# Kernel tuning notes

Measured on AMD Instinct MI355X. Metric: run time of the kernel, lower is better.

Reference implementation:

```python
import jax, jax.numpy as jnp
import numpy as np

B, T, V, EMB, H = 16, 128, 32000, 512, 512
PAD = 0


def setup_inputs() -> dict:
    key = jax.random.key(0)
    ks = jax.random.split(key, 20)
    s = 0.02
    inp = {
        "X": jax.random.randint(ks[0], (B, T + 1), 0, V),
        "mask": jnp.zeros((T, T), dtype=bool),
        "encoder_outputs": jax.random.normal(ks[1], (B, T, H), jnp.float32),
        "embedding": jax.random.normal(ks[2], (V, EMB), jnp.float32) * s,
        "W_ih0": jax.random.normal(ks[3], (4 * H, EMB), jnp.float32) * s,
        "W_hh0": jax.random.normal(ks[4], (4 * H, H), jnp.float32) * s,
        "b_ih0": jnp.zeros((4 * H,), jnp.float32),
        "b_hh0": jnp.zeros((4 * H,), jnp.float32),
        "W_ih1": jax.random.normal(ks[5], (4 * H, H), jnp.float32) * s,
        "W_hh1": jax.random.normal(ks[6], (4 * H, H), jnp.float32) * s,
        "b_ih1": jnp.zeros((4 * H,), jnp.float32),
        "b_hh1": jnp.zeros((4 * H,), jnp.float32),
        "attn_W": jax.random.normal(ks[7], (H, 2 * H), jnp.float32) * s,
        "attn_b": jnp.zeros((H,), jnp.float32),
        "v_w": jax.random.normal(ks[8], (H,), jnp.float32) * s,
        "fc_W": jax.random.normal(ks[9], (V, 2 * H), jnp.float32) * s,
        "fc_b": jnp.zeros((V,), jnp.float32),
        "h0": jax.random.normal(ks[10], (2, B, H), jnp.float32) * 0.01,
        "c0": jax.random.normal(ks[11], (2, B, H), jnp.float32) * 0.01,
    }
    return inp


def _lstm_cell(x, h, c, Wi, Wh, bi, bh):
    # torch LSTM gate order: i, f, g, o
    g = x @ Wi.T + h @ Wh.T + bi + bh
    i, f, gg, o = jnp.split(g, 4, axis=-1)
    c2 = jax.nn.sigmoid(f) * c + jax.nn.sigmoid(i) * jnp.tanh(gg)
    h2 = jax.nn.sigmoid(o) * jnp.tanh(c2)
    return h2, c2


def reference(X, mask, encoder_outputs, embedding,
              W_ih0, W_hh0, b_ih0, b_hh0,
              W_ih1, W_hh1, b_ih1, b_hh1,
              attn_W, attn_b, v_w, fc_W, fc_b, h0, c0):
    Hd = h0.shape[-1]
    E = embedding[X[:, :-1]]            # [B, T, EMB]
    xs = jnp.swapaxes(E, 0, 1)          # [T, B, EMB]

    def step(carry, x_t):
        h, c = carry                    # each [2, B, H]
        h0n, c0n = _lstm_cell(x_t, h[0], c[0], W_ih0, W_hh0, b_ih0, b_hh0)
        h1n, c1n = _lstm_cell(h0n, h[1], c[1], W_ih1, W_hh1, b_ih1, b_hh1)
        return (jnp.stack([h0n, h1n]), jnp.stack([c0n, c1n])), h1n

    _, H_all = jax.lax.scan(step, (h0, c0), xs)   # [T, B, H] top-layer hiddens

    # Bahdanau attention (vectorized over t since it only depends on h_t, mask[t])
    Wh, We = attn_W[:, :Hd], attn_W[:, Hd:]
    ph = jnp.einsum('tbh,kh->tbk', H_all, Wh)              # [T, B, H]
    pe = jnp.einsum('blh,kh->blk', encoder_outputs, We)    # [B, L, H]
    energy = jnp.tanh(ph[:, :, None, :] + pe[None] + attn_b)  # [T, B, L, H]
    logits = jnp.einsum('tblk,k->tbl', energy, v_w)        # [T, B, L]
    logits = jnp.where(mask[:, None, :], jnp.float32(-1e9), logits)
    # Faithful to source: softmax over dim=1 of the broadcast [1,B,L] tensor,
    # i.e. normalization over the BATCH axis.
    att = jax.nn.softmax(logits, axis=1)                   # [T, B, L]
    weighted = jnp.einsum('tbl,blh->tbh', att, encoder_outputs)  # [T, B, H]

    out = jnp.concatenate([H_all, weighted], axis=-1) @ fc_W.T + fc_b  # [T, B, V]
    Z = jnp.swapaxes(out, 0, 1).reshape(-1, fc_b.shape[0])  # [B*T, V]
    Y = X[:, 1:].reshape(-1)                                # [B*T]

    logp = jax.nn.log_softmax(Z, axis=-1)
    nll = -jnp.take_along_axis(logp, Y[:, None], axis=1)[:, 0]
    valid = (Y != PAD).astype(logp.dtype)
    return jnp.sum(nll * valid) / jnp.sum(valid)
```

## Files before the change

### kernel.cpp

```cpp
#include <hip/hip_runtime.h>


#define DI __device__ __forceinline__

typedef __attribute__((ext_vector_type(8))) short short8;
typedef __attribute__((ext_vector_type(4))) float floatx4;
typedef unsigned long long ull;

#define TSEQ   128
#define VOCAB  32000
#define GDIM   2048
#define NROW   2048
#define KFC    1024
#define HPAD   520

DI float bf2f(unsigned short u) {
    union { unsigned u; float f; } x; x.u = ((unsigned)u) << 16; return x.f;
}
DI unsigned short f2bf(float f) {
    unsigned u = __float_as_uint(f);
    unsigned r = (u + 0x7FFF + ((u >> 16) & 1)) >> 16;
    return (unsigned short)r;
}
DI short8 ld8(const unsigned short* p) { return *(const short8*)p; }
DI floatx4 mfma16(short8 a, short8 b, floatx4 c) {
    return __builtin_amdgcn_mfma_f32_16x16x32_bf16(a, b, c, 0, 0, 0);
}
DI float sigm(float x) { return __builtin_amdgcn_rcpf(1.f + __expf(-x)); }
DI float tanh_f(float x) {
    float xc = fminf(8.f, fmaxf(-8.f, x));
    float e  = __expf(2.f * xc);
    return (e - 1.f) * __builtin_amdgcn_rcpf(e + 1.f);
}

#define GLD16(gsrc, ldst)                                                     \
    __builtin_amdgcn_global_load_lds(                                         \
        (const __attribute__((address_space(1))) unsigned int*)(gsrc),        \
        (__attribute__((address_space(3))) unsigned int*)(ldst), 16, 0, 0)

__global__ void zero_out_kernel(float* out, int n) {
    int i = blockIdx.x * 64 + threadIdx.x;
    if (i < n) out[i] = 0.f;
}

__global__ void prep_kernel(const int* X, const float* enc, const float* emb,
                            const float* Wih0, const float* Whh0,
                            const float* Wih1, const float* Whh1,
                            const float* attnW, const float* h0,
                            const float* fcW,
                            unsigned short* wih0b, unsigned short* whh0b,
                            unsigned short* wih1b, unsigned short* whh1b,
                            unsigned short* whb, unsigned short* web,
                            unsigned short* encb, unsigned short* enctb,
                            unsigned short* xsb,
                            unsigned short* h0buf, unsigned short* h1buf,
                            unsigned short* fcWb,
                            int* ctrl) {
    if (blockIdx.x == 0) {
#pragma unroll
        for (int j = 0; j < 12; ++j) ctrl[threadIdx.x + 256 * j] = 0;
    }
    long i = (long)blockIdx.x * 256 + threadIdx.x;
    const long NW = 1048576;
    const long NA = 262144;
    if (i < NW) { wih0b[i] = f2bf(Wih0[i]); return; } i -= NW;
    if (i < NW) { whh0b[i] = f2bf(Whh0[i]); return; } i -= NW;
    if (i < NW) { wih1b[i] = f2bf(Wih1[i]); return; } i -= NW;
    if (i < NW) { whh1b[i] = f2bf(Whh1[i]); return; } i -= NW;
    if (i < NA) { long k = i >> 9, h = i & 511; whb[i] = f2bf(attnW[k * 1024 + h]);       return; } i -= NA;
    if (i < NA) { long k = i >> 9, h = i & 511; web[i] = f2bf(attnW[k * 1024 + 512 + h]); return; } i -= NA;
    if (i < NW) { encb[i] = f2bf(enc[i]); return; } i -= NW;
    if (i < NW) {
        long b = i >> 16, r = i & 65535, h = r >> 7, l = r & 127;
        enctb[i] = f2bf(enc[(b * 128 + l) * 512 + h]); return;
    } i -= NW;
    if (i < NW) {
        long m = i >> 9, e = i & 511, t = m >> 4, b = m & 15;
        int xi = X[b * 129 + t];
        xi = (xi < 0) ? 0 : ((xi >= VOCAB) ? VOCAB - 1 : xi);
        xsb[i] = f2bf(emb[(long)xi * 512 + e]); return;
    } i -= NW;
    if (i < 16384) {
        long layer = i >> 13, r = i & 8191;
        unsigned short v = f2bf(h0[layer * 8192 + r]);
        if (layer == 0) h0buf[8192 + r] = v; else h1buf[8192 + r] = v;
        return;
    } i -= 16384;
    if (i < 8192000) {
        float4 v = ((const float4*)fcW)[i];
        ushort4 o;
        o.x = f2bf(v.x); o.y = f2bf(v.y); o.z = f2bf(v.z); o.w = f2bf(v.w);
        ((ushort4*)fcWb)[i] = o;
    }
}

DI void gemm64_acc(const unsigned short* A, const unsigned short* Bw,
                   int m0, int n0, int lda, int ldb, int nkb, floatx4 acc[4]) {
    int tid = threadIdx.x;
    int wv = tid >> 6, ln = tid & 63;
    int colL = ln & 15, koff = (ln >> 4) * 8;
    const unsigned short* ar  = A  + (size_t)(m0 + wv * 16 + colL) * lda + koff;
    const unsigned short* br0 = Bw + (size_t)(n0 +  0 + colL) * ldb + koff;
    const unsigned short* br1 = Bw + (size_t)(n0 + 16 + colL) * ldb + koff;
    const unsigned short* br2 = Bw + (size_t)(n0 + 32 + colL) * ldb + koff;
    const unsigned short* br3 = Bw + (size_t)(n0 + 48 + colL) * ldb + koff;
    for (int kb = 0; kb < nkb; ++kb) {
        short8 af = ld8(ar + kb * 32);
        acc[0] = mfma16(af, ld8(br0 + kb * 32), acc[0]);
        acc[1] = mfma16(af, ld8(br1 + kb * 32), acc[1]);
        acc[2] = mfma16(af, ld8(br2 + kb * 32), acc[2]);
        acc[3] = mfma16(af, ld8(br3 + kb * 32), acc[3]);
    }
}

__global__ void a0_kernel(const unsigned short* xs, const unsigned short* wih0b,
                          const float* bih0, const float* bhh0, unsigned short* A0b) {
    floatx4 acc[4] = {{0,0,0,0},{0,0,0,0},{0,0,0,0},{0,0,0,0}};
    int m0 = blockIdx.x * 64, n0 = blockIdx.y * 64;
    gemm64_acc(xs, wih0b, m0, n0, 512, 512, 16, acc);
    int tid = threadIdx.x, wv = tid >> 6, ln = tid & 63, colL = ln & 15, q = ln >> 4;
    int mrow = m0 + wv * 16;
#pragma unroll
    for (int nt = 0; nt < 4; ++nt) {
        int col = n0 + nt * 16 + colL;
        float bb = bih0[col] + bhh0[col];
#pragma unroll
        for (int r = 0; r < 4; ++r)
            A0b[(size_t)(mrow + q * 4 + r) * GDIM + col] = f2bf(acc[nt][r] + bb);
    }
}

__global__ __launch_bounds__(512, 1)
void lstm_kernel(const unsigned short* A0b,
                 const unsigned short* whh0b, const unsigned short* wih1b,
                 const unsigned short* whh1b,
                 const float* bih1, const float* bhh1, const float* c0in,
                 unsigned short* h0buf, unsigned short* h1buf,
                 unsigned short* Hall, unsigned short* Gmat, int* flags) {
    __shared__ unsigned short hsh0[16 * HPAD];
    __shared__ unsigned short hsh1[16 * HPAD];
    __shared__ float gbuf[2][4][16][16];
    int wg = blockIdx.x;
    int tid = threadIdx.x;
    int half = tid >> 8;
    int lt   = tid & 255;
    int wv = lt >> 6, ln = lt & 63;
    int u0 = wg * 16;
    int n0 = wv * 512 + u0;
    int colL = ln & 15, q = ln >> 4, koff = q * 8;
    int eb = lt >> 4, eu = lt & 15;
    float c = c0in[half * 8192 + eb * 512 + u0 + eu];
    float bias1 = (half == 1) ? (bih1[n0 + colL] + bhh1[n0 + colL]) : 0.f;

    short8 wA[16], wB[16];
    if (half == 0) {
        const unsigned short* wr0 = whh0b + (size_t)(n0 + colL) * 512 + koff;
#pragma unroll
        for (int kb = 0; kb < 16; ++kb) wA[kb] = ld8(wr0 + kb * 32);
#pragma unroll
        for (int kb = 0; kb < 16; ++kb) wB[kb] = wA[kb];
    } else {
        const unsigned short* wr1 = wih1b + (size_t)(n0 + colL) * 512 + koff;
        const unsigned short* wr2 = whh1b + (size_t)(n0 + colL) * 512 + koff;
#pragma unroll
        for (int kb = 0; kb < 16; ++kb) wA[kb] = ld8(wr1 + kb * 32);
#pragma unroll
        for (int kb = 0; kb < 16; ++kb) wB[kb] = ld8(wr2 + kb * 32);
    }

    floatx4 a0pre = {0, 0, 0, 0};
    if (half == 0) {
        const unsigned short* a0r = A0b + (size_t)0 * GDIM + n0 + colL;
        a0pre[0] = bf2f(a0r[(q * 4 + 0) * GDIM]);
        a0pre[1] = bf2f(a0r[(q * 4 + 1) * GDIM]);
        a0pre[2] = bf2f(a0r[(q * 4 + 2) * GDIM]);
        a0pre[3] = bf2f(a0r[(q * 4 + 3) * GDIM]);
    }

    int srow = tid >> 5;
    int scol = (tid & 31) << 4;
    unsigned long long* d0 = (unsigned long long*)&hsh0[srow * HPAD + scol];
    unsigned long long* d1 = (unsigned long long*)&hsh1[srow * HPAD + scol];

#pragma unroll 1
    for (int t = 0; t <= TSEQ; ++t) {
        bool actL0 = (t < TSEQ);
        bool actL1 = (t >= 1);
        {
            const unsigned long long* s0 =
                (const unsigned long long*)(h0buf + ((t - 1) & 1) * 8192) + (size_t)tid * 4;
            unsigned long long v0 = __hip_atomic_load(s0 + 0, __ATOMIC_RELAXED, __HIP_MEMORY_SCOPE_AGENT);
            unsigned long long v1 = __hip_atomic_load(s0 + 1, __ATOMIC_RELAXED, __HIP_MEMORY_SCOPE_AGENT);
            unsigned long long v2 = __hip_atomic_load(s0 + 2, __ATOMIC_RELAXED, __HIP_MEMORY_SCOPE_AGENT);
            unsigned long long v3 = __hip_atomic_load(s0 + 3, __ATOMIC_RELAXED, __HIP_MEMORY_SCOPE_AGENT);
            if (actL1) {
                const unsigned long long* s1 =
                    (const unsigned long long*)(h1buf + ((t - 2) & 1) * 8192) + (size_t)tid * 4;
                unsigned long long w0 = __hip_atomic_load(s1 + 0, __ATOMIC_RELAXED, __HIP_MEMORY_SCOPE_AGENT);
                unsigned long long w1 = __hip_atomic_load(s1 + 1, __ATOMIC_RELAXED, __HIP_MEMORY_SCOPE_AGENT);
                unsigned long long w2 = __hip_atomic_load(s1 + 2, __ATOMIC_RELAXED, __HIP_MEMORY_SCOPE_AGENT);
                unsigned long long w3 = __hip_atomic_load(s1 + 3, __ATOMIC_RELAXED, __HIP_MEMORY_SCOPE_AGENT);
                d0[0] = v0; d0[1] = v1; d0[2] = v2; d0[3] = v3;
                d1[0] = w0; d1[1] = w1; d1[2] = w2; d1[3] = w3;
            } else {
                d0[0] = v0; d0[1] = v1; d0[2] = v2; d0[3] = v3;
            }
        }
        __syncthreads();
        bool act = half ? actL1 : actL0;
        if (act) {
            floatx4 acc;
            const unsigned short* hl0 = hsh0 + colL * HPAD + koff;
            if (half == 0) {
                acc = a0pre;
#pragma unroll
                for (int kb = 0; kb < 16; ++kb)
                    acc = mfma16(ld8(hl0 + kb * 32), wA[kb], acc);
            } else {
                acc[0] = bias1; acc[1] = bias1; acc[2] = bias1; acc[3] = bias1;
                const unsigned short* hl1 = hsh1 + colL * HPAD + koff;
#pragma unroll
                for (int kb = 0; kb < 16; ++kb)
                    acc = mfma16(ld8(hl0 + kb * 32), wA[kb], acc);
#pragma unroll
                for (int kb = 0; kb < 16; ++kb)
                    acc = mfma16(ld8(hl1 + kb * 32), wB[kb], acc);
            }
            gbuf[half][wv][q * 4 + 0][colL] = acc[0];
            gbuf[half][wv][q * 4 + 1][colL] = acc[1];
            gbuf[half][wv][q * 4 + 2][colL] = acc[2];
            gbuf[half][wv][q * 4 + 3][colL] = acc[3];
        }
        __syncthreads();
        if (act) {
            float gi = gbuf[half][0][eb][eu], gf = gbuf[half][1][eb][eu];
            float gg = gbuf[half][2][eb][eu], go = gbuf[half][3][eb][eu];
            float c2 = sigm(gf) * c + sigm(gi) * tanh_f(gg);
            float h2 = sigm(go) * tanh_f(c2);
            c = c2;
            unsigned hb = (unsigned)f2bf(h2);
            unsigned up = __shfl_down(hb, 1, 64);
            unsigned packed = hb | (up << 16);
            if ((eu & 1) == 0) {
                if (half == 0) {
                    __hip_atomic_store(
                        (unsigned*)(h0buf + (t & 1) * 8192 + eb * 512 + u0 + eu),
                        packed, __ATOMIC_RELAXED, __HIP_MEMORY_SCOPE_AGENT);
                } else {
                    int s = t - 1;
                    __hip_atomic_store(
                        (unsigned*)(h1buf + (s & 1) * 8192 + eb * 512 + u0 + eu),
                        packed, __ATOMIC_RELAXED, __HIP_MEMORY_SCOPE_AGENT);
                    *(unsigned*)&Hall[(size_t)(s * 16 + eb) * 512 + u0 + eu] = packed;
                    *(unsigned*)&Gmat[(size_t)(eb * 128 + s) * KFC + u0 + eu] = packed;
                }
            }
        }
        if (t < TSEQ) {
            __syncthreads();
            if (tid == 0)
                __hip_atomic_store(flags + wg * 32, t + 1,
                                   __ATOMIC_RELAXED, __HIP_MEMORY_SCOPE_AGENT);
            if (half == 0 && t + 1 < TSEQ) {
                const unsigned short* a0r = A0b + (size_t)((t + 1) * 16) * GDIM + n0 + colL;
                a0pre[0] = bf2f(a0r[(q * 4 + 0) * GDIM]);
                a0pre[1] = bf2f(a0r[(q * 4 + 1) * GDIM]);
                a0pre[2] = bf2f(a0r[(q * 4 + 2) * GDIM]);
                a0pre[3] = bf2f(a0r[(q * 4 + 3) * GDIM]);
            }
            if (tid < 32) {
                int guard = 0;
                while (__hip_atomic_load(flags + tid * 32, __ATOMIC_RELAXED,
                                         __HIP_MEMORY_SCOPE_AGENT) < t + 1) {
                    __builtin_amdgcn_s_sleep(1);
                    if (++guard > (1 << 22)) break;
                }
            }
            __syncthreads();
        }
    }
}

__global__ void phpe_kernel(const unsigned short* Hall, const unsigned short* encb,
                            const unsigned short* whb, const unsigned short* web,
                            const float* attnb, float* ph, float* pe) {
    bool ispe = (blockIdx.z != 0);
    const unsigned short* A  = ispe ? encb : Hall;
    const unsigned short* Bw = ispe ? web  : whb;
    float* out = ispe ? pe : ph;
    floatx4 acc[4] = {{0,0,0,0},{0,0,0,0},{0,0,0,0},{0,0,0,0}};
    int m0 = blockIdx.x * 64, n0 = blockIdx.y * 64;
    gemm64_acc(A, Bw, m0, n0, 512, 512, 16, acc);
    int tid = threadIdx.x, wv = tid >> 6, ln = tid & 63, colL = ln & 15, q = ln >> 4;
    int mrow = m0 + wv * 16;
#pragma unroll
    for (int nt = 0; nt < 4; ++nt) {
        int col = n0 + nt * 16 + colL;
        float bb = ispe ? attnb[col] : 0.f;
#pragma unroll
        for (int r = 0; r < 4; ++r)
            out[(size_t)(mrow + q * 4 + r) * 512 + col] = acc[nt][r] + bb;
    }
}

__global__ void logits_kernel(const float* ph, const float* pe, const float* vw,
                              float* logits) {
    int m = blockIdx.x;
    int t = m >> 4, b = m & 15;
    int tid = threadIdx.x, wv = tid >> 6, ln = tid & 63;
    const float* phr = ph + (size_t)m * 512 + ln * 8;
    floatx4 ph0 = *(const floatx4*)phr;
    floatx4 ph1 = *(const floatx4*)(phr + 4);
    const float* vwr = vw + ln * 8;
    floatx4 vw0 = *(const floatx4*)vwr;
    floatx4 vw1 = *(const floatx4*)(vwr + 4);
    for (int li = 0; li < 32; ++li) {
        int ll = wv * 32 + li;
        const float* per = pe + (size_t)(b * 128 + ll) * 512 + ln * 8;
        floatx4 p0 = *(const floatx4*)per;
        floatx4 p1 = *(const floatx4*)(per + 4);
        float s = 0.f;
#pragma unroll
        for (int j = 0; j < 4; ++j) s += vw0[j] * tanh_f(ph0[j] + p0[j]);
#pragma unroll
        for (int j = 0; j < 4; ++j) s += vw1[j] * tanh_f(ph1[j] + p1[j]);
#pragma unroll
        for (int off = 32; off; off >>= 1) s += __shfl_xor(s, off, 64);
        if (ln == 0) logits[((size_t)t * 128 + ll) * 16 + b] = s;
    }
}

__global__ void att_kernel(const float* logits, unsigned short* attb) {
    int t = blockIdx.x, l = threadIdx.x;
    const float* p = logits + ((size_t)t * 128 + l) * 16;
    float x[16], mx = -1e30f;
#pragma unroll
    for (int j = 0; j < 16; ++j) { x[j] = p[j]; mx = fmaxf(mx, x[j]); }
    float s = 0.f;
#pragma unroll
    for (int j = 0; j < 16; ++j) { x[j] = __expf(x[j] - mx); s += x[j]; }
    float inv = __builtin_amdgcn_rcpf(s);
#pragma unroll
    for (int j = 0; j < 16; ++j)
        attb[((size_t)j * 128 + t) * 128 + l] = f2bf(x[j] * inv);
}

__global__ void weighted_kernel(const unsigned short* attb, const unsigned short* enctb,
                                unsigned short* Gmat) {
    int b = blockIdx.z;
    floatx4 acc[4] = {{0,0,0,0},{0,0,0,0},{0,0,0,0},{0,0,0,0}};
    int m0 = blockIdx.x * 64, n0 = blockIdx.y * 64;
    gemm64_acc(attb + (size_t)b * 128 * 128, enctb + (size_t)b * 512 * 128,
               m0, n0, 128, 128, 4, acc);
    int tid = threadIdx.x, wv = tid >> 6, ln = tid & 63, colL = ln & 15, q = ln >> 4;
    int mrow = m0 + wv * 16;
#pragma unroll
    for (int nt = 0; nt < 4; ++nt) {
        int col = n0 + nt * 16 + colL;
#pragma unroll
        for (int r = 0; r < 4; ++r)
            Gmat[(size_t)(b * 128 + mrow + q * 4 + r) * KFC + 512 + col] = f2bf(acc[nt][r]);
    }
}

__global__ __launch_bounds__(256)
void fc_kernel(const unsigned short* G, const unsigned short* fcWb,
               const float* fcb, float2* partials) {
    __shared__ __align__(16) unsigned short lA[128 * 64];
    __shared__ __align__(16) unsigned short lB[128 * 64];
    __shared__ float2 pbuf[128][2];
    int nwg = blockIdx.x;
    int mwg = blockIdx.y;
    int n_base = nwg * 128, m_base = mwg * 128;
    int tid = threadIdx.x, wv = tid >> 6, l = tid & 63;
    int wr = wv >> 1, wc = wv & 1;
    int colL = l & 15, q16 = l >> 4, koff = q16 * 8;
    int srow = l >> 3, scol = (l & 7) * 8;

    floatx4 acc[4][4];
#pragma unroll
    for (int i = 0; i < 4; ++i)
#pragma unroll
        for (int j = 0; j < 4; ++j) acc[i][j] = (floatx4){0, 0, 0, 0};

    const unsigned short* gA = G    + (size_t)m_base * KFC;
    const unsigned short* gB = fcWb + (size_t)n_base * KFC;

    for (int kt = 0; kt < 16; ++kt) {
        if (kt) __syncthreads();
        int k0 = kt * 64;
#pragma unroll
        for (int j = 0; j < 4; ++j) {
            int c = wv * 4 + j;
            const unsigned short* ga = gA + (size_t)(c * 8 + srow) * KFC + k0 + scol;
            const unsigned short* gb = gB + (size_t)(c * 8 + srow) * KFC + k0 + scol;
            GLD16(ga, lA + c * 512);
            GLD16(gb, lB + c * 512);
        }
        __syncthreads();
#pragma unroll
        for (int ks = 0; ks < 2; ++ks) {
            const unsigned short* ap = lA + (wr * 64 + colL) * 64 + ks * 32 + koff;
            const unsigned short* bp = lB + (wc * 64 + colL) * 64 + ks * 32 + koff;
            short8 aF[4], bF[4];
#pragma unroll
            for (int ma = 0; ma < 4; ++ma) aF[ma] = ld8(ap + ma * 16 * 64);
#pragma unroll
            for (int nb = 0; nb < 4; ++nb) bF[nb] = ld8(bp + nb * 16 * 64);
#pragma unroll
            for (int ma = 0; ma < 4; ++ma)
#pragma unroll
                for (int nb = 0; nb < 4; ++nb)
                    acc[ma][nb] = mfma16(aF[ma], bF[nb], acc[ma][nb]);
        }
    }

    float cb[4];
#pragma unroll
    for (int nb = 0; nb < 4; ++nb)
        cb[nb] = fcb[n_base + wc * 64 + nb * 16 + colL];

#pragma unroll
    for (int ma = 0; ma < 4; ++ma) {
#pragma unroll
        for (int r = 0; r < 4; ++r) {
            float v0 = acc[ma][0][r] + cb[0];
            float v1 = acc[ma][1][r] + cb[1];
            float v2 = acc[ma][2][r] + cb[2];
            float v3 = acc[ma][3][r] + cb[3];
            float M = fmaxf(fmaxf(v0, v1), fmaxf(v2, v3));
#pragma unroll
            for (int off = 1; off < 16; off <<= 1) M = fmaxf(M, __shfl_xor(M, off, 64));
            float e = __expf(v0 - M) + __expf(v1 - M) + __expf(v2 - M) + __expf(v3 - M);
#pragma unroll
            for (int off = 1; off < 16; off <<= 1) e += __shfl_xor(e, off, 64);
            if (colL == 0)
                pbuf[wr * 64 + ma * 16 + q16 * 4 + r][wc] = make_float2(M, e);
        }
    }
    __syncthreads();
    if (tid < 128) {
        float2 a = pbuf[tid][0], b = pbuf[tid][1];
        float M = fmaxf(a.x, b.x);
        float S = a.y * __expf(a.x - M) + b.y * __expf(b.x - M);
        partials[(size_t)(m_base + tid) * 250 + nwg] = make_float2(M, S);
    }
}

__global__ void tgt_kernel(const unsigned short* G, const float* fcW, const float* fcb,
                           const int* X, float* tgt) {
    int r = blockIdx.x * 4 + (threadIdx.x >> 6);
    int ln = threadIdx.x & 63;
    int b = r >> 7, t = r & 127;
    int y = X[b * 129 + t + 1];
    y = (y < 0) ? 0 : ((y >= VOCAB) ? VOCAB - 1 : y);
    const unsigned short* g = G + (size_t)r * KFC;
    const float* w = fcW + (size_t)y * KFC;
    float s = 0.f;
    for (int j = ln; j < KFC; j += 64) s += bf2f(g[j]) * w[j];
#pragma unroll
    for (int off = 32; off; off >>= 1) s += __shfl_xor(s, off, 64);
    if (ln == 0) tgt[r] = s + fcb[y];
}

__global__ void row_lse_kernel(const float2* partials, float* lse) {
    int row = blockIdx.x * 8 + (threadIdx.x >> 5);
    int ln = threadIdx.x & 31;
    const float2* p = partials + (size_t)row * 250;
    float M = -1e30f, S = 0.f;
    for (int i = ln; i < 250; i += 32) {
        float2 q = p[i];
        float nm = fmaxf(M, q.x);
        S = S * __expf(M - nm) + q.y * __expf(q.x - nm);
        M = nm;
    }
#pragma unroll
    for (int off = 16; off; off >>= 1) {
        float Mo = __shfl_xor(M, off, 64);
        float So = __shfl_xor(S, off, 64);
        float nm = fmaxf(M, Mo);
        S = S * __expf(M - nm) + So * __expf(Mo - nm);
        M = nm;
    }
    if (ln == 0) lse[row] = M + __logf(S);
}

__global__ void finalize2_kernel(const float* lse, const float* tgt,
                                 const int* X, float* out) {
    int tid = threadIdx.x;
    float vs = 0.f, vc = 0.f;
    for (int r = tid; r < NROW; r += 256) {
        int b = r >> 7, t = r & 127;
        int y = X[b * 129 + t + 1];
        if (y != 0) { vs += lse[r] - tgt[r]; vc += 1.f; }
    }
    __shared__ float sv[256], sc[256];
    sv[tid] = vs; sc[tid] = vc;
    __syncthreads();
    for (int s = 128; s; s >>= 1) {
        if (tid < s) { sv[tid] += sv[tid + s]; sc[tid] += sc[tid + s]; }
        __syncthreads();
    }
    if (tid == 0) out[0] = sv[0] / sc[0];
}

extern "C" void kernel_launch(void* const* d_in, const int* in_sizes, int n_in,
                              void* d_out, int out_size, void* d_ws, size_t ws_size,
                              hipStream_t stream) {
    const int*   X     = (const int*)d_in[0];
    const float* enc   = (const float*)d_in[2];
    const float* emb   = (const float*)d_in[3];
    const float* Wih0  = (const float*)d_in[4];
    const float* Whh0  = (const float*)d_in[5];
    const float* bih0  = (const float*)d_in[6];
    const float* bhh0  = (const float*)d_in[7];
    const float* Wih1  = (const float*)d_in[8];
    const float* Whh1  = (const float*)d_in[9];
    const float* bih1  = (const float*)d_in[10];
    const float* bhh1  = (const float*)d_in[11];
    const float* attnW = (const float*)d_in[12];
    const float* attnb = (const float*)d_in[13];
    const float* vw    = (const float*)d_in[14];
    const float* fcW   = (const float*)d_in[15];
    const float* fcb   = (const float*)d_in[16];
    const float* h0    = (const float*)d_in[17];
    const float* c0    = (const float*)d_in[18];

    char* ws = (char*)d_ws;
    size_t off = 0;
    auto take = [&](size_t bytes) { char* p = ws + off; off += (bytes + 255) & ~(size_t)255; return p; };
    int*            ctrl    = (int*)           take(12288);
    unsigned short* wih0b   = (unsigned short*)take(2097152);
    unsigned short* whh0b   = (unsigned short*)take(2097152);
    unsigned short* wih1b   = (unsigned short*)take(2097152);
    unsigned short* whh1b   = (unsigned short*)take(2097152);
    unsigned short* whb     = (unsigned short*)take(524288);
    unsigned short* web     = (unsigned short*)take(524288);
    unsigned short* encb    = (unsigned short*)take(2097152);
    unsigned short* enctb   = (unsigned short*)take(2097152);
    unsigned short* xsb     = (unsigned short*)take(2097152);
    unsigned short* h0buf   = (unsigned short*)take(32768);
    unsigned short* h1buf   = (unsigned short*)take(32768);
    unsigned short* A0b     = (unsigned short*)take(8388608);
    unsigned short* hallb   = (unsigned short*)take(2097152);
    unsigned short* gmat    = (unsigned short*)take(4194304);
    float*          ph      = (float*)         take(4194304);
    float*          pe      = (float*)         take(4194304);
    float*          logitsb = (float*)         take(1048576);
    unsigned short* attb    = (unsigned short*)take(524288);
    float2*         parts   = (float2*)        take(4096000);
    float*          tgt     = (float*)         take(8192);
    float*          lseb    = (float*)         take(8192);
    unsigned short* fcWb    = (unsigned short*)take(65536000);
    size_t need = off;
    (void)in_sizes; (void)n_in;

    if (ws_size < need) {
        hipLaunchKernelGGL(zero_out_kernel, dim3((out_size + 63) / 64), dim3(64),
                           0, stream, (float*)d_out, out_size);
        return;
    }

    hipLaunchKernelGGL(prep_kernel, dim3(62784), dim3(256), 0, stream,
                       X, enc, emb, Wih0, Whh0, Wih1, Whh1, attnW, h0, fcW,
                       wih0b, whh0b, wih1b, whh1b, whb, web, encb, enctb,
                       xsb, h0buf, h1buf, fcWb, ctrl);
    hipLaunchKernelGGL(a0_kernel, dim3(32, 32), dim3(256), 0, stream,
                       xsb, wih0b, bih0, bhh0, A0b);
    hipLaunchKernelGGL(lstm_kernel, dim3(32), dim3(512), 0, stream,
                       A0b, whh0b, wih1b, whh1b, bih1, bhh1, c0,
                       h0buf, h1buf, hallb, gmat, ctrl);
    hipLaunchKernelGGL(phpe_kernel, dim3(32, 8, 2), dim3(256), 0, stream,
                       hallb, encb, whb, web, attnb, ph, pe);
    hipLaunchKernelGGL(logits_kernel, dim3(2048), dim3(256), 0, stream,
                       ph, pe, vw, logitsb);
    hipLaunchKernelGGL(att_kernel, dim3(128), dim3(128), 0, stream,
                       logitsb, attb);
    hipLaunchKernelGGL(weighted_kernel, dim3(2, 8, 16), dim3(256), 0, stream,
                       attb, enctb, gmat);
    hipLaunchKernelGGL(fc_kernel, dim3(250, 16), dim3(256), 0, stream,
                       gmat, fcWb, fcb, parts);
    hipLaunchKernelGGL(tgt_kernel, dim3(512), dim3(256), 0, stream,
                       gmat, fcW, fcb, X, tgt);
    hipLaunchKernelGGL(row_lse_kernel, dim3(256), dim3(256), 0, stream,
                       parts, lseb);
    hipLaunchKernelGGL(finalize2_kernel, dim3(1), dim3(256), 0, stream,
                       lseb, tgt, X, (float*)d_out);
}
```

Measured before the change: 1.044 ms.

## Overlap fc weight bf16 conversion with LSTM recurrence using extra blocks

Moves the fp32-to-bf16 conversion of the large fc weight matrix out of the prep kernel into 224 extra workgroups launched alongside the 32 LSTM workgroups, so the bandwidth-bound conversion runs while the latency-bound recurrence executes. It also changes the per-step barrier: all threads now poll the flags directly instead of 32 threads polling followed by a __syncthreads. Risks include the extra blocks competing for memory bandwidth and CU slots with the spin-waiting LSTM blocks (launch_bounds 512,1), possible scheduling issues if LSTM blocks are not co-resident, and a weaker ordering of shared-memory reads after removing the trailing barrier.

```diff
diff --git a/kernel.cpp b/kernel.cpp
--- a/kernel.cpp
+++ b/kernel.cpp
@@ -47,14 +47,12 @@
                             const float* Wih0, const float* Whh0,
                             const float* Wih1, const float* Whh1,
                             const float* attnW, const float* h0,
-                            const float* fcW,
                             unsigned short* wih0b, unsigned short* whh0b,
                             unsigned short* wih1b, unsigned short* whh1b,
                             unsigned short* whb, unsigned short* web,
                             unsigned short* encb, unsigned short* enctb,
                             unsigned short* xsb,
                             unsigned short* h0buf, unsigned short* h1buf,
-                            unsigned short* fcWb,
                             int* ctrl) {
     if (blockIdx.x == 0) {
 #pragma unroll
@@ -84,13 +82,6 @@
         long layer = i >> 13, r = i & 8191;
         unsigned short v = f2bf(h0[layer * 8192 + r]);
         if (layer == 0) h0buf[8192 + r] = v; else h1buf[8192 + r] = v;
-        return;
-    } i -= 16384;
-    if (i < 8192000) {
-        float4 v = ((const float4*)fcW)[i];
-        ushort4 o;
-        o.x = f2bf(v.x); o.y = f2bf(v.y); o.z = f2bf(v.z); o.w = f2bf(v.w);
-        ((ushort4*)fcWb)[i] = o;
     }
 }
 
@@ -136,12 +127,26 @@
                  const unsigned short* whh1b,
                  const float* bih1, const float* bhh1, const float* c0in,
                  unsigned short* h0buf, unsigned short* h1buf,
-                 unsigned short* Hall, unsigned short* Gmat, int* flags) {
+                 unsigned short* Hall, unsigned short* Gmat, int* flags,
+                 const float* fcW, unsigned short* fcWb) {
+    int wg = blockIdx.x;
+    int tid = threadIdx.x;
+
+    if (wg >= 32) {
+        const float4* src = (const float4*)fcW;
+        ushort4* dst = (ushort4*)fcWb;
+        for (long i = (long)(wg - 32) * 512 + tid; i < 8192000; i += 224 * 512) {
+            float4 v = src[i];
+            ushort4 o;
+            o.x = f2bf(v.x); o.y = f2bf(v.y); o.z = f2bf(v.z); o.w = f2bf(v.w);
+            dst[i] = o;
+        }
+        return;
+    }
+
     __shared__ unsigned short hsh0[16 * HPAD];
     __shared__ unsigned short hsh1[16 * HPAD];
     __shared__ float gbuf[2][4][16][16];
-    int wg = blockIdx.x;
-    int tid = threadIdx.x;
     int half = tid >> 8;
     int lt   = tid & 255;
     int wv = lt >> 6, ln = lt & 63;
@@ -268,15 +273,16 @@
                 a0pre[2] = bf2f(a0r[(q * 4 + 2) * GDIM]);
                 a0pre[3] = bf2f(a0r[(q * 4 + 3) * GDIM]);
             }
-            if (tid < 32) {
-                int guard = 0;
-                while (__hip_atomic_load(flags + tid * 32, __ATOMIC_RELAXED,
+            {
+                int* f = flags + (tid & 31) * 32;
+                int g = 0;
+                while (__hip_atomic_load(f, __ATOMIC_RELAXED,
                                          __HIP_MEMORY_SCOPE_AGENT) < t + 1) {
                     __builtin_amdgcn_s_sleep(1);
-                    if (++guard > (1 << 22)) break;
+                    if (++g > (1 << 22)) break;
                 }
+                asm volatile("" ::: "memory");
             }
-            __syncthreads();
         }
     }
 }
@@ -561,15 +567,15 @@
         return;
     }
 
-    hipLaunchKernelGGL(prep_kernel, dim3(62784), dim3(256), 0, stream,
-                       X, enc, emb, Wih0, Whh0, Wih1, Whh1, attnW, h0, fcW,
+    hipLaunchKernelGGL(prep_kernel, dim3(30784), dim3(256), 0, stream,
+                       X, enc, emb, Wih0, Whh0, Wih1, Whh1, attnW, h0,
                        wih0b, whh0b, wih1b, whh1b, whb, web, encb, enctb,
-                       xsb, h0buf, h1buf, fcWb, ctrl);
+                       xsb, h0buf, h1buf, ctrl);
     hipLaunchKernelGGL(a0_kernel, dim3(32, 32), dim3(256), 0, stream,
                        xsb, wih0b, bih0, bhh0, A0b);
-    hipLaunchKernelGGL(lstm_kernel, dim3(32), dim3(512), 0, stream,
+    hipLaunchKernelGGL(lstm_kernel, dim3(256), dim3(512), 0, stream,
                        A0b, whh0b, wih1b, whh1b, bih1, bhh1, c0,
-                       h0buf, h1buf, hallb, gmat, ctrl);
+                       h0buf, h1buf, hallb, gmat, ctrl, fcW, fcWb);
     hipLaunchKernelGGL(phpe_kernel, dim3(32, 8, 2), dim3(256), 0, stream,
                        hallb, encb, whb, web, attnb, ph, pe);
     hipLaunchKernelGGL(logits_kernel, dim3(2048), dim3(256), 0, stream,
```

New measurement: 988.1 us. -5.4%, faster.
